# Kernel optimization log

Measured on AMD Instinct MI355X. Metric: run time of the kernel, lower is better.

The kernel has to match this reference:

```python
import jax, jax.numpy as jnp
import numpy as np

K = 12           # boundary_k
TEMP = 0.75      # logit_temperature


def _knn_idx(p):
    # p: [N,3]; brute-force kNN within one batch element (pointops offsets => per-batch)
    sq = jnp.sum(p * p, axis=-1)
    d2 = sq[:, None] + sq[None, :] - 2.0 * (p @ p.T)   # [N,N]
    _, idx = jax.lax.top_k(-d2, K + 1)                  # self is nearest (d=0)
    return idx[:, 1:]                                    # drop self -> [N,K]


def _mlp2(x, W1, b1, W2, b2, relu_out):
    h = jax.nn.relu(x @ W1 + b1) @ W2 + b2
    return jax.nn.relu(h) if relu_out else h


def setup_inputs() -> dict:
    key = jax.random.key(0)
    ks = jax.random.split(key, 32)
    B, N, C = 4, 4096, 17
    dims = [256, 512, 768]
    RD = 320
    s = 0.02
    inp = {
        'feat0': jax.random.normal(ks[0], (B, N, dims[0]), jnp.float32),
        'feat1': jax.random.normal(ks[1], (B, N, dims[1]), jnp.float32),
        'feat2': jax.random.normal(ks[2], (B, N, dims[2]), jnp.float32),
        'logits': jax.random.normal(ks[3], (B, N, C), jnp.float32),
        'labels': jax.random.randint(ks[4], (B, N), 0, C, jnp.int32),
        'pos': jax.random.normal(ks[5], (B, N, 3), jnp.float32),
    }
    # feat projections
    for i, d in enumerate(dims):
        inp[f'Wp{i}'] = jax.random.normal(ks[6 + i], (d, RD), jnp.float32) * s
        inp[f'bp{i}'] = jnp.zeros((RD,), jnp.float32)
    # boundary encoder 6->96->160
    inp['Wbe1'] = jax.random.normal(ks[10], (6, 96), jnp.float32) * s
    inp['bbe1'] = jnp.zeros((96,), jnp.float32)
    inp['Wbe2'] = jax.random.normal(ks[11], (96, 160), jnp.float32) * s
    inp['bbe2'] = jnp.zeros((160,), jnp.float32)
    # attention (RD+160)->320->n_scales
    inp['Wa1'] = jax.random.normal(ks[12], (RD + 160, 320), jnp.float32) * s
    inp['ba1'] = jnp.zeros((320,), jnp.float32)
    inp['Wa2'] = jax.random.normal(ks[13], (320, 3), jnp.float32) * s
    inp['ba2'] = jnp.zeros((3,), jnp.float32)
    # output proj RD->RD->RD
    inp['Wo1'] = jax.random.normal(ks[14], (RD, RD), jnp.float32) * s
    inp['bo1'] = jnp.zeros((RD,), jnp.float32)
    inp['Wo2'] = jax.random.normal(ks[15], (RD, RD), jnp.float32) * s
    inp['bo2'] = jnp.zeros((RD,), jnp.float32)
    return inp


def boundary_info(logits, labels, pos):
    idx = jax.vmap(_knn_idx)(pos)                          # [B,N,K]
    nb_lab = jax.vmap(lambda l, i: l[i])(labels, idx)      # [B,N,K]
    nb_pos = jax.vmap(lambda p, i: p[i])(pos, idx)         # [B,N,K,3]
    diff = nb_lab != labels[..., None]                     # [B,N,K]
    diff_f = diff.astype(jnp.float32)
    dist = jnp.linalg.norm(nb_pos - pos[:, :, None, :], axis=-1)  # [B,N,K]
    boundary_score = diff_f.mean(axis=-1)
    same = 1.0 - diff_f
    same_dist = (dist * same).sum(-1) / (same.sum(-1) + 1e-6)
    bdist = jnp.min(jnp.where(diff, dist, jnp.inf), axis=-1)
    bdist = jnp.where(jnp.isfinite(bdist), bdist, same_dist)
    mean_d = dist.mean(-1)
    density = 1.0 / (mean_d + 1e-6)
    curvature = jnp.std(dist, axis=-1, ddof=1) / (mean_d + 1e-6)  # torch.std unbiased
    probs = jax.nn.softmax(logits / TEMP, axis=-1)
    confidence = probs.max(-1)
    entropy = -(probs * jnp.log(probs + 1e-8)).sum(-1) / jnp.log(jnp.float32(probs.shape[-1]))
    return jnp.stack([boundary_score, confidence, entropy, density, curvature, bdist], axis=-1)


def reference(feat0, feat1, feat2, logits, labels, pos,
              Wp0, bp0, Wp1, bp1, Wp2, bp2,
              Wbe1, bbe1, Wbe2, bbe2,
              Wa1, ba1, Wa2, ba2,
              Wo1, bo1, Wo2, bo2):
    fp = jnp.stack([feat0 @ Wp0 + bp0, feat1 @ Wp1 + bp1, feat2 @ Wp2 + bp2], axis=2)  # [B,N,3,RD]
    info = boundary_info(logits, labels, pos)                       # [B,N,6]
    enc = _mlp2(info, Wbe1, bbe1, Wbe2, bbe2, relu_out=True)        # [B,N,160]
    global_feat = fp.mean(axis=2)                                   # [B,N,RD]
    attn_in = jnp.concatenate([global_feat, enc], axis=-1)
    attn = jax.nn.softmax(_mlp2(attn_in, Wa1, ba1, Wa2, ba2, relu_out=False), axis=-1)  # [B,N,3]
    fused = (fp * attn[..., None]).sum(axis=2)                      # [B,N,RD]
    out = _mlp2(fused, Wo1, bo1, Wo2, bo2, relu_out=False) + global_feat
    return out, attn
```

## Files before the change

kernel.cpp:

```cpp
#include <hip/hip_runtime.h>
#include <stdint.h>

typedef float fx4 __attribute__((ext_vector_type(4)));
typedef short s8 __attribute__((ext_vector_type(8)));
typedef short s4 __attribute__((ext_vector_type(4)));
typedef unsigned int u32;
typedef u32 ux4 __attribute__((ext_vector_type(4)));

#define MTOT 16384
#define NPTS 4096

#define VMCNT3 asm volatile("s_waitcnt vmcnt(3)" ::: "memory")
#define VMCNT2 asm volatile("s_waitcnt vmcnt(2)" ::: "memory")
#define VMCNT0 asm volatile("s_waitcnt vmcnt(0)" ::: "memory")
#define LGKM0  asm volatile("s_waitcnt lgkmcnt(0)" ::: "memory")
#define SBAR   asm volatile("s_barrier" ::: "memory")
#define SCHED0 __builtin_amdgcn_sched_barrier(0)

__device__ __forceinline__ float b2f(short s) {
    return __uint_as_float(((unsigned)(unsigned short)s) << 16);
}
__device__ __forceinline__ short f2b(float f) {
    unsigned u = __float_as_uint(f);
    u += 0x7fffu + ((u >> 16) & 1u);
    return (short)(u >> 16);
}
__device__ __forceinline__ void g2l16(const void* g, void* l) {
    __builtin_amdgcn_global_load_lds(
        (const __attribute__((address_space(1))) unsigned int*)g,
        (__attribute__((address_space(3))) unsigned int*)l, 16, 0, 0);
}
__device__ __forceinline__ void g2l4(const void* g, void* l) {
    __builtin_amdgcn_global_load_lds(
        (const __attribute__((address_space(1))) unsigned int*)g,
        (__attribute__((address_space(3))) unsigned int*)l, 4, 0, 0);
}

struct WTDesc {
    const float* W[8];
    short* Bt[8];
    int K[8];
    int N[8];
    int Kp[8];
    int swz[8];
    int base[9];
};

__global__ __launch_bounds__(256) void wtrans8_kernel(WTDesc d)
{
    int idx = blockIdx.x * 256 + threadIdx.x;
    if (idx >= d.base[8]) return;
    int s = 0;
#pragma unroll
    for (int t = 1; t < 8; ++t) if (idx >= d.base[t]) s = t;
    int local = idx - d.base[s];
    int N = d.N[s];
    if (d.swz[s]) {
        int c = local / 10240, r = local - c * 10240;
        int n = r >> 5, q = r & 31, slot = q >> 3, t = q & 7;
        int kl = ((slot ^ ((n >> 1) & 3)) << 3) | t;
        int k = c * 32 + kl;
        d.Bt[s][local] = f2b(d.W[s][(size_t)k * N + n]);
    } else {
        int Kp = d.Kp[s], K = d.K[s];
        int n = local / Kp, k = local - n * Kp;
        d.Bt[s][local] = (k < K) ? f2b(d.W[s][(size_t)k * N + n]) : (short)0;
    }
}

#define SEGW 132
#define KCAP 40

__global__ __launch_bounds__(512) void knap_kernel(
    const float* __restrict__ pos, u32* __restrict__ keys,
    const float* __restrict__ f0, const float* __restrict__ f1, const float* __restrict__ f2,
    short* __restrict__ a0, short* __restrict__ a1, short* __restrict__ a2)
{
    __shared__ float xs[8 * SEGW], ys[8 * SEGW], zs[8 * SEGW];
    __shared__ u32 cand[64 * KCAP];
    __shared__ u32 samp[64 * 16];
    __shared__ u32 tauA[64];
    __shared__ int cnt[64];

    if (blockIdx.x >= 1024) {
        int g = (blockIdx.x - 1024) * 512 + threadIdx.x;
        const float* src; short* dst; int K; size_t w;
        if (g < 1572864)      { src = f2; dst = a2; K = 768; w = (size_t)g * 8; }
        else if (g < 2621440) { src = f1; dst = a1; K = 512; w = (size_t)(g - 1572864) * 8; }
        else                  { src = f0; dst = a0; K = 256; w = (size_t)(g - 2621440) * 8; }
        int Kt = K * 64;
        int mtile = (int)(w / (size_t)Kt);
        int r2 = (int)(w - (size_t)mtile * Kt);
        int chunk = r2 >> 11;
        int within = r2 & 2047;
        int r = within >> 5, q = within & 31;
        int slot = q >> 3;
        int k = chunk * 32 + ((slot ^ ((r >> 1) & 3)) << 3);
        int row = mtile * 64 + r;
        const float* sp = src + (size_t)row * K + k;
        fx4 v0 = *(const fx4*)sp, v1 = *(const fx4*)(sp + 4);
        s8 o;
        o[0] = f2b(v0[0]); o[1] = f2b(v0[1]); o[2] = f2b(v0[2]); o[3] = f2b(v0[3]);
        o[4] = f2b(v1[0]); o[5] = f2b(v1[1]); o[6] = f2b(v1[2]); o[7] = f2b(v1[3]);
        *(s8*)(dst + w) = o;
        return;
    }

    int bid = blockIdx.x;
    int b   = bid >> 8;
    int cc  = (bid >> 6) & 3;
    int pch = bid & 63;
    int tid = threadIdx.x;
    int jb  = cc << 10;

    if (tid < 64) cnt[tid] = 0;
    for (int idx = tid; idx < 1024; idx += 512) {
        int seg = idx >> 7, o = idx & 127;
        const float* pp = pos + (size_t)(b * NPTS + jb + idx) * 3;
        xs[seg * SEGW + o] = pp[0];
        ys[seg * SEGW + o] = pp[1];
        zs[seg * SEGW + o] = pp[2];
    }
    __syncthreads();

    int lp = tid >> 3, q = tid & 7;
    int gi = pch * 64 + lp;
    const float* mp = pos + (size_t)(b * NPTS + gi) * 3;
    float mx = mp[0], my = mp[1], mz = mp[2];

    const float* xsq = xs + q * SEGW;
    const float* ysq = ys + q * SEGW;
    const float* zsq = zs + q * SEGW;
    int jg0 = jb + q * 128;

    u32 h0 = 0xFFFFFFFFu, h1v = 0xFFFFFFFFu;
    for (int jj = 0; jj < 128; jj += 4) {
        fx4 xv = *reinterpret_cast<const fx4*>(xsq + jj);
        fx4 yv = *reinterpret_cast<const fx4*>(ysq + jj);
        fx4 zv = *reinterpret_cast<const fx4*>(zsq + jj);
#pragma unroll
        for (int u = 0; u < 4; ++u) {
            float dx = xv[u] - mx, dy = yv[u] - my, dz = zv[u] - mz;
            float d2 = fmaf(dx, dx, fmaf(dy, dy, dz * dz));
            int jg = jg0 + jj + u;
            u32 key = (__float_as_uint(d2) & 0xFFFFF000u) | (u32)jg;
            if (jg == gi) key = 0xFFFFFFFFu;
            u32 lo = (key < h0) ? key : h0;
            u32 hi = (key < h0) ? h0 : key;
            h0 = lo;
            h1v = (hi < h1v) ? hi : h1v;
        }
    }
    samp[lp * 16 + q * 2]     = h0;
    samp[lp * 16 + q * 2 + 1] = h1v;
    __syncthreads();

    {
        ux4 sv0 = *(ux4*)&samp[lp * 16];
        ux4 sv1 = *(ux4*)&samp[lp * 16 + 4];
        ux4 sv2 = *(ux4*)&samp[lp * 16 + 8];
        ux4 sv3 = *(ux4*)&samp[lp * 16 + 12];
        int r0 = 0, r1 = 0;
#pragma unroll
        for (int i = 0; i < 4; ++i) {
            r0 += (sv0[i] < h0) + (sv1[i] < h0) + (sv2[i] < h0) + (sv3[i] < h0);
            r1 += (sv0[i] < h1v) + (sv1[i] < h1v) + (sv2[i] < h1v) + (sv3[i] < h1v);
        }
        if (r0 == 11) tauA[lp] = h0;
        if (r1 == 11) tauA[lp] = h1v;
    }
    __syncthreads();
    u32 tau = tauA[lp];

    for (int jj = 0; jj < 128; jj += 4) {
        fx4 xv = *reinterpret_cast<const fx4*>(xsq + jj);
        fx4 yv = *reinterpret_cast<const fx4*>(ysq + jj);
        fx4 zv = *reinterpret_cast<const fx4*>(zsq + jj);
#pragma unroll
        for (int u = 0; u < 4; ++u) {
            float dx = xv[u] - mx, dy = yv[u] - my, dz = zv[u] - mz;
            float d2 = fmaf(dx, dx, fmaf(dy, dy, dz * dz));
            int jg = jg0 + jj + u;
            u32 key = (__float_as_uint(d2) & 0xFFFFF000u) | (u32)jg;
            if (jg == gi) key = 0xFFFFFFFFu;
            if (key <= tau) {
                int slot = atomicAdd(&cnt[lp], 1);
                if (slot < KCAP) cand[lp * KCAP + slot] = key;
            }
        }
    }
    __syncthreads();

    int n = cnt[lp];
    u32 out[12];
    if (n <= KCAP) {
        u32 e0, e1, e2, e3, e4;
        e0 = (q      < n) ? cand[lp * KCAP + q]      : 0xFFFFFFFFu;
        e1 = (q + 8  < n) ? cand[lp * KCAP + q + 8]  : 0xFFFFFFFFu;
        e2 = (q + 16 < n) ? cand[lp * KCAP + q + 16] : 0xFFFFFFFFu;
        e3 = (q + 24 < n) ? cand[lp * KCAP + q + 24] : 0xFFFFFFFFu;
        e4 = (q + 32 < n) ? cand[lp * KCAP + q + 32] : 0xFFFFFFFFu;
#define CE(a, b) { u32 t0 = (a < b) ? a : b; u32 t1 = (a < b) ? b : a; a = t0; b = t1; }
        CE(e0, e1) CE(e1, e2) CE(e2, e3) CE(e3, e4)
        CE(e0, e1) CE(e1, e2) CE(e2, e3)
        CE(e0, e1) CE(e1, e2)
        CE(e0, e1)
#undef CE
        cand[lp * KCAP + q]      = e0;
        cand[lp * KCAP + q + 8]  = e1;
        cand[lp * KCAP + q + 16] = e2;
        cand[lp * KCAP + q + 24] = e3;
        cand[lp * KCAP + q + 32] = e4;
        int ptr = 0;
        u32 head = e0;
#pragma unroll
        for (int r = 0; r < 12; ++r) {
            u32 m = head;
            u32 o1 = __shfl_xor(m, 4, 8); m = (o1 < m) ? o1 : m;
            u32 o2 = __shfl_xor(m, 2, 8); m = (o2 < m) ? o2 : m;
            u32 o3 = __shfl_xor(m, 1, 8); m = (o3 < m) ? o3 : m;
            if (m == head) {
                ++ptr;
                head = (ptr < 5) ? cand[lp * KCAP + q + ptr * 8] : 0xFFFFFFFFu;
            }
            out[r] = m;
        }
    } else {
        u32 hk[12];
#pragma unroll
        for (int k = 0; k < 12; ++k) hk[k] = 0xFFFFFFFFu;
        for (int jj = 0; jj < 128; jj += 4) {
            fx4 xv = *reinterpret_cast<const fx4*>(xsq + jj);
            fx4 yv = *reinterpret_cast<const fx4*>(ysq + jj);
            fx4 zv = *reinterpret_cast<const fx4*>(zsq + jj);
#pragma unroll
            for (int u = 0; u < 4; ++u) {
                float dx = xv[u] - mx, dy = yv[u] - my, dz = zv[u] - mz;
                float d2 = fmaf(dx, dx, fmaf(dy, dy, dz * dz));
                int jg = jg0 + jj + u;
                u32 key = (__float_as_uint(d2) & 0xFFFFF000u) | (u32)jg;
                if (jg == gi) key = 0xFFFFFFFFu;
                if (key < hk[11]) {
                    hk[11] = key;
#pragma unroll
                    for (int k = 11; k >= 1; --k) {
                        u32 a = hk[k], bb = hk[k - 1];
                        u32 mn = (a < bb) ? a : bb;
                        u32 mxv = (a < bb) ? bb : a;
                        hk[k - 1] = mn; hk[k] = mxv;
                    }
                }
            }
        }
#pragma unroll
        for (int r = 0; r < 12; ++r) {
            u32 m = hk[0];
            u32 o1 = __shfl_xor(m, 4, 8); m = (o1 < m) ? o1 : m;
            u32 o2 = __shfl_xor(m, 2, 8); m = (o2 < m) ? o2 : m;
            u32 o3 = __shfl_xor(m, 1, 8); m = (o3 < m) ? o3 : m;
            if (m == hk[0]) {
#pragma unroll
                for (int k = 0; k < 11; ++k) hk[k] = hk[k + 1];
                hk[11] = 0xFFFFFFFFu;
            }
            out[r] = m;
        }
    }

    size_t kb = ((size_t)(b * NPTS + gi) * 4 + cc) * 12;
    if (q == 0) *reinterpret_cast<ux4*>(&keys[kb])     = (ux4){out[0], out[1], out[2], out[3]};
    if (q == 1) *reinterpret_cast<ux4*>(&keys[kb + 4]) = (ux4){out[4], out[5], out[6], out[7]};
    if (q == 2) *reinterpret_cast<ux4*>(&keys[kb + 8]) = (ux4){out[8], out[9], out[10], out[11]};
}

__global__ __launch_bounds__(256) void knn_merge_kernel(
    const u32* __restrict__ keys, const int* __restrict__ labels,
    const float* __restrict__ logits, float* __restrict__ info32)
{
    __shared__ unsigned char labs[NPTS];
    int b  = blockIdx.x >> 6;
    int pc = blockIdx.x & 63;
    int tid = threadIdx.x;
    for (int idx = tid; idx < NPTS; idx += 256)
        labs[idx] = (unsigned char)labels[b * NPTS + idx];
    __syncthreads();

    int lp = tid >> 2, q = tid & 3;
    int gi = pc * 64 + lp;
    size_t kb = ((size_t)(b * NPTS + gi) * 4 + q) * 12;
    ux4 k0 = *reinterpret_cast<const ux4*>(&keys[kb]);
    ux4 k1 = *reinterpret_cast<const ux4*>(&keys[kb + 4]);
    ux4 k2 = *reinterpret_cast<const ux4*>(&keys[kb + 8]);
    u32 hk[12];
    hk[0] = k0[0]; hk[1] = k0[1]; hk[2] = k0[2]; hk[3] = k0[3];
    hk[4] = k1[0]; hk[5] = k1[1]; hk[6] = k1[2]; hk[7] = k1[3];
    hk[8] = k2[0]; hk[9] = k2[1]; hk[10] = k2[2]; hk[11] = k2[3];

    int mylab = (int)labs[gi];
    float sum_d = 0.f, sum_d2 = 0.f, sum_diff = 0.f, same_d = 0.f, bmin = 3.0e38f;
#pragma unroll
    for (int r = 0; r < 12; ++r) {
        u32 m = hk[0];
        u32 o1 = __shfl_xor(m, 2, 4); m = (o1 < m) ? o1 : m;
        u32 o2 = __shfl_xor(m, 1, 4); m = (o2 < m) ? o2 : m;
        if (m == hk[0]) {
#pragma unroll
            for (int k = 0; k < 11; ++k) hk[k] = hk[k + 1];
            hk[11] = 0xFFFFFFFFu;
        }
        float d = sqrtf(__uint_as_float(m & 0xFFFFF000u));
        int j = (int)(m & 0xFFFu);
        float isdiff = ((int)labs[j] != mylab) ? 1.0f : 0.0f;
        sum_d += d;
        sum_d2 = fmaf(d, d, sum_d2);
        sum_diff += isdiff;
        same_d = fmaf(d, 1.0f - isdiff, same_d);
        if (isdiff > 0.f) bmin = fminf(bmin, d);
    }

    if (q == 0) {
        float nsame = 12.0f - sum_diff;
        float mean_d = sum_d * (1.0f / 12.0f);
        float var = fmaxf(0.f, (sum_d2 - 12.0f * mean_d * mean_d) * (1.0f / 11.0f));
        float md_eps = mean_d + 1e-6f;
        float curvature = sqrtf(var) / md_eps;
        float density = 1.0f / md_eps;
        float same_dist = same_d / (nsame + 1e-6f);
        float bdist = (bmin < 2.9e38f) ? bmin : same_dist;
        float bscore = sum_diff * (1.0f / 12.0f);

        const float* lg = logits + (size_t)(b * NPTS + gi) * 17;
        float v[17];
        float vmax = -3.0e38f;
#pragma unroll
        for (int c = 0; c < 17; ++c) { v[c] = lg[c] * (1.0f / 0.75f); vmax = fmaxf(vmax, v[c]); }
        float ssum = 0.f;
#pragma unroll
        for (int c = 0; c < 17; ++c) { v[c] = expf(v[c] - vmax); ssum += v[c]; }
        float inv = 1.0f / ssum;
        float conf = 0.f, ent = 0.f;
#pragma unroll
        for (int c = 0; c < 17; ++c) {
            float pprob = v[c] * inv;
            conf = fmaxf(conf, pprob);
            ent += pprob * logf(pprob + 1e-8f);
        }
        ent = -ent * (1.0f / 2.8332133f);

        float* op = info32 + (size_t)(b * NPTS + gi) * 32;
        fx4 o0 = {bscore, conf, ent, density};
        fx4 o1v = {curvature, bdist, 0.f, 0.f};
        fx4 zz = {0.f, 0.f, 0.f, 0.f};
        *reinterpret_cast<fx4*>(op + 0)  = o0;
        *reinterpret_cast<fx4*>(op + 4)  = o1v;
        *reinterpret_cast<fx4*>(op + 8)  = zz;
        *reinterpret_cast<fx4*>(op + 12) = zz;
        *reinterpret_cast<fx4*>(op + 16) = zz;
        *reinterpret_cast<fx4*>(op + 20) = zz;
        *reinterpret_cast<fx4*>(op + 24) = zz;
        *reinterpret_cast<fx4*>(op + 28) = zz;
    }
}

template<bool AF32, bool RELU, bool NMASK, bool ADDF, bool OUTF, bool OUTB>
__global__ __launch_bounds__(256) void gemm_k(
    const void* __restrict__ Ap, int lda,
    const short* __restrict__ Bt,
    const float* __restrict__ bias,
    float* __restrict__ Cf, int ldcf,
    short* __restrict__ Cb, int ldcb, int cboff,
    const float* __restrict__ Af, int ldaf,
    int N, int K, int ntiles)
{
    __shared__ short As[128 * 40];
    __shared__ short Bs[64 * 40];
    int bid = blockIdx.x;
    int mt = bid / ntiles, nt = bid - mt * ntiles;
    int m0 = mt * 128, n0 = nt * 64;
    int tid = threadIdx.x, l = tid & 63, wid = tid >> 6;
    int wm = wid & 1, wn = wid >> 1, lr = l & 15, lh = l >> 4;
    fx4 acc[4][2] = {};

    int nsteps = K >> 5;
    for (int kt = 0; kt < nsteps; ++kt) {
        int k0 = kt << 5;
        if constexpr (AF32) {
            const float* A = (const float*)Ap;
#pragma unroll
            for (int it = 0; it < 4; ++it) {
                int tt = tid + it * 256;
                int row = tt >> 3, seg = tt & 7;
                fx4 vv = *reinterpret_cast<const fx4*>(A + (size_t)(m0 + row) * lda + k0 + seg * 4);
                s4 w; w[0] = f2b(vv[0]); w[1] = f2b(vv[1]); w[2] = f2b(vv[2]); w[3] = f2b(vv[3]);
                *reinterpret_cast<s4*>(&As[row * 40 + seg * 4]) = w;
            }
        } else {
            const short* A = (const short*)Ap;
#pragma unroll
            for (int it = 0; it < 2; ++it) {
                int tt = tid + it * 256;
                int row = tt >> 2, seg = tt & 3;
                s8 vv = *reinterpret_cast<const s8*>(A + (size_t)(m0 + row) * lda + k0 + seg * 8);
                *reinterpret_cast<s8*>(&As[row * 40 + seg * 8]) = vv;
            }
        }
        {
            int row = tid >> 2, seg = tid & 3;
            s8 vb = {0, 0, 0, 0, 0, 0, 0, 0};
            if (!NMASK || (n0 + row) < N)
                vb = *reinterpret_cast<const s8*>(Bt + (size_t)(n0 + row) * K + k0 + seg * 8);
            *reinterpret_cast<s8*>(&Bs[row * 40 + seg * 8]) = vb;
        }
        __syncthreads();
        s8 af[4], bfr[2];
#pragma unroll
        for (int mf = 0; mf < 4; ++mf)
            af[mf] = *reinterpret_cast<s8*>(&As[(wm * 64 + mf * 16 + lr) * 40 + lh * 8]);
#pragma unroll
        for (int nf = 0; nf < 2; ++nf)
            bfr[nf] = *reinterpret_cast<s8*>(&Bs[(wn * 32 + nf * 16 + lr) * 40 + lh * 8]);
#pragma unroll
        for (int mf = 0; mf < 4; ++mf)
#pragma unroll
            for (int nf = 0; nf < 2; ++nf)
                acc[mf][nf] = __builtin_amdgcn_mfma_f32_16x16x32_bf16(af[mf], bfr[nf], acc[mf][nf], 0, 0, 0);
        __syncthreads();
    }

#pragma unroll
    for (int nf = 0; nf < 2; ++nf) {
        int col = n0 + wn * 32 + nf * 16 + lr;
        if (NMASK && col >= N) continue;
        float bv = bias[col];
#pragma unroll
        for (int mf = 0; mf < 4; ++mf) {
            int r0 = m0 + wm * 64 + mf * 16 + lh * 4;
#pragma unroll
            for (int rg = 0; rg < 4; ++rg) {
                float c = acc[mf][nf][rg] + bv;
                if (RELU) c = fmaxf(c, 0.0f);
                int row = r0 + rg;
                if constexpr (ADDF) c += Af[(size_t)row * ldaf + col];
                if constexpr (OUTF) Cf[(size_t)row * ldcf + col] = c;
                if constexpr (OUTB) Cb[(size_t)row * ldcb + cboff + col] = f2b(c);
            }
        }
    }
}

__global__ __launch_bounds__(1024, 1) void mega_kernel(
    const short* __restrict__ at0, const short* __restrict__ at1, const short* __restrict__ at2,
    const short* __restrict__ btp0, const short* __restrict__ btp1, const short* __restrict__ btp2,
    const float* __restrict__ bp0, const float* __restrict__ bp1, const float* __restrict__ bp2,
    const short* __restrict__ bta1, const float* __restrict__ ba1,
    const float* __restrict__ Wa2, const float* __restrict__ ba2,
    const short* __restrict__ bto1, const float* __restrict__ bo1,
    const short* __restrict__ bto2, const float* __restrict__ bo2,
    const short* __restrict__ encb,
    float* __restrict__ outf, float* __restrict__ attn_out)
{
    __shared__ alignas(16) char smb[136192];
    const int BBo[3] = {0, 20480, 40960};
    const int ABo[3] = {61440, 65536, 69632};
    constexpr int R2B = 73728, SWF = 135168;
    float* smf = (float*)(smb + SWF);

    int tid = threadIdx.x, wid = tid >> 6, l = tid & 63;
    int wm = wid >> 2, wn = wid & 3, lr = l & 15, lh = l >> 4;
    int m0 = blockIdx.x * 64;

    auto stageB = [&](int bbase, const short* btg, int kt) {
        const char* s = (const char*)(btg + (size_t)kt * 10240);
        int o1 = tid * 16;
        int o2 = 16384 + tid * 4;
        g2l16(s + o1, smb + bbase + o1);
        g2l4(s + o2, smb + bbase + o2);
    };
    auto stageA = [&](int abase, const short* atgm, int kt) {
        const char* s = (const char*)(atgm + (size_t)kt * 2048);
        g2l4(s + tid * 4, smb + abase + tid * 4);
    };
    auto readB = [&](int bbase, s8* bf) {
#pragma unroll
        for (int nf = 0; nf < 5; ++nf) {
            int row = wn * 80 + nf * 16 + lr;
            bf[nf] = *(const s8*)(smb + bbase + row * 64 + ((lh ^ ((row >> 1) & 3)) << 4));
        }
    };

    fx4 gacc[5] = {};

    auto do_proj = [&](const short* atgm, const short* btg, int ns,
                       const float* bias, s4 (&fpks)[5]) {
        fx4 acc[5] = {};
        stageB(BBo[0], btg, 0); stageA(ABo[0], atgm, 0);
        stageB(BBo[1], btg, 1); stageA(ABo[1], atgm, 1);
        LGKM0;
#pragma unroll 1
        for (int kt = 0; kt < ns; ++kt) {
            if (kt < ns - 1) { VMCNT3; } else { VMCNT0; }
            SBAR;
            int ph = kt - (kt / 3) * 3;
            s8 af, bf[5];
            {
                int row = wm * 16 + lr;
                af = *(const s8*)(smb + ABo[ph] + row * 64 + ((lh ^ ((row >> 1) & 3)) << 4));
            }
            readB(BBo[ph], bf);
            if (kt + 2 < ns) {
                int p2 = (kt + 2) - ((kt + 2) / 3) * 3;
                stageB(BBo[p2], btg, kt + 2);
                stageA(ABo[p2], atgm, kt + 2);
            }
#pragma unroll
            for (int nf = 0; nf < 5; ++nf)
                acc[nf] = __builtin_amdgcn_mfma_f32_16x16x32_bf16(af, bf[nf], acc[nf], 0, 0, 0);
            SCHED0; LGKM0;
        }
        SBAR;
#pragma unroll
        for (int nf = 0; nf < 5; ++nf) {
            float bv = bias[wn * 80 + nf * 16 + lr];
            s4 pk;
#pragma unroll
            for (int rg = 0; rg < 4; ++rg) {
                float c = acc[nf][rg] + bv;
                gacc[nf][rg] += c;
                pk[rg] = f2b(c);
            }
            fpks[nf] = pk;
        }
    };

    s4 fpk0[5], fpk1[5], fpk2[5];
    do_proj(at2 + (size_t)blockIdx.x * 49152, btp2, 24, bp2, fpk2);
    do_proj(at1 + (size_t)blockIdx.x * 32768, btp1, 16, bp1, fpk1);
    do_proj(at0 + (size_t)blockIdx.x * 16384, btp0, 8,  bp0, fpk0);

    s4 gh[5];
#pragma unroll
    for (int nf = 0; nf < 5; ++nf) {
        int col = wn * 80 + nf * 16 + lr;
        s4 pk;
#pragma unroll
        for (int rg = 0; rg < 4; ++rg) {
            int row = wm * 16 + lh * 4 + rg;
            short gs = f2b(gacc[nf][rg] * (1.0f / 3.0f));
            pk[rg] = gs;
            int bir = (col * 2) ^ (((row >> 1) & 3) << 4);
            *(short*)(smb + R2B + row * 960 + bir) = gs;
        }
        gh[nf] = pk;
    }
#pragma unroll
    for (int r = 0; r < 2; ++r) {
        int idx = tid + r * 1024;
        if (idx < 1280) {
            int row = idx / 20, sg = idx - row * 20;
            s8 v = *reinterpret_cast<const s8*>(encb + (size_t)(m0 + row) * 160 + sg * 8);
            int bir = (640 + sg * 16) ^ (((row >> 1) & 3) << 4);
            *(s8*)(smb + R2B + row * 960 + bir) = v;
        }
    }

    auto do_gemm2 = [&](const short* btg, int ns, fx4 (&acc)[5]) {
        stageB(BBo[0], btg, 0);
        stageB(BBo[1], btg, 1);
        LGKM0;
#pragma unroll 1
        for (int kt = 0; kt < ns; ++kt) {
            if (kt < ns - 1) { VMCNT2; } else { VMCNT0; }
            SBAR;
            int ph = kt - (kt / 3) * 3;
            s8 af, bf[5];
            {
                int row = wm * 16 + lr;
                int bir = (kt * 64 + (lh << 4)) ^ (((row >> 1) & 3) << 4);
                af = *(const s8*)(smb + R2B + row * 960 + bir);
            }
            readB(BBo[ph], bf);
            if (kt + 2 < ns) {
                int p2 = (kt + 2) - ((kt + 2) / 3) * 3;
                stageB(BBo[p2], btg, kt + 2);
            }
#pragma unroll
            for (int nf = 0; nf < 5; ++nf)
                acc[nf] = __builtin_amdgcn_mfma_f32_16x16x32_bf16(af, bf[nf], acc[nf], 0, 0, 0);
            SCHED0; LGKM0;
        }
        SBAR;
    };

    {
        fx4 acc1[5] = {};
        do_gemm2(bta1, 15, acc1);
#pragma unroll
        for (int nf = 0; nf < 5; ++nf) {
            int col = wn * 80 + nf * 16 + lr;
            float bv = ba1[col];
#pragma unroll
            for (int rg = 0; rg < 4; ++rg) {
                int row = wm * 16 + lh * 4 + rg;
                int bir = (col * 2) ^ (((row >> 1) & 3) << 4);
                *(short*)(smb + R2B + row * 960 + bir) = f2b(fmaxf(acc1[nf][rg] + bv, 0.0f));
            }
        }
    }

    {
        float* ws2 = (float*)smb;
        if (tid < 240)
            reinterpret_cast<fx4*>(ws2)[tid] = reinterpret_cast<const fx4*>(Wa2)[tid];
        __syncthreads();
        if (tid < 512) {
            int row = tid >> 3, g = tid & 7;
            float l0 = 0.f, l1 = 0.f, l2 = 0.f;
#pragma unroll
            for (int j = 0; j < 5; ++j) {
                int bir = (g * 80 + j * 16) ^ (((row >> 1) & 3) << 4);
                s8 v = *(const s8*)(smb + R2B + row * 960 + bir);
#pragma unroll
                for (int u = 0; u < 8; ++u) {
                    float f = b2f(v[u]);
                    const float* wp = ws2 + (g * 40 + j * 8 + u) * 3;
                    l0 = fmaf(f, wp[0], l0);
                    l1 = fmaf(f, wp[1], l1);
                    l2 = fmaf(f, wp[2], l2);
                }
            }
#pragma unroll
            for (int s = 4; s >= 1; s >>= 1) {
                l0 += __shfl_xor(l0, s, 8);
                l1 += __shfl_xor(l1, s, 8);
                l2 += __shfl_xor(l2, s, 8);
            }
            if (g == 0) {
                l0 += ba2[0]; l1 += ba2[1]; l2 += ba2[2];
                float mx = fmaxf(l0, fmaxf(l1, l2));
                float e0 = expf(l0 - mx), e1 = expf(l1 - mx), e2 = expf(l2 - mx);
                float inv = 1.0f / (e0 + e1 + e2);
                float w0 = e0 * inv, w1 = e1 * inv, w2 = e2 * inv;
                attn_out[(size_t)(m0 + row) * 3 + 0] = w0;
                attn_out[(size_t)(m0 + row) * 3 + 1] = w1;
                attn_out[(size_t)(m0 + row) * 3 + 2] = w2;
                smf[row * 4 + 0] = w0; smf[row * 4 + 1] = w1; smf[row * 4 + 2] = w2;
            }
        }
        __syncthreads();
    }

#pragma unroll
    for (int rg = 0; rg < 4; ++rg) {
        int row = wm * 16 + lh * 4 + rg;
        float w0 = smf[row * 4 + 0], w1 = smf[row * 4 + 1], w2 = smf[row * 4 + 2];
#pragma unroll
        for (int nf = 0; nf < 5; ++nf) {
            int col = wn * 80 + nf * 16 + lr;
            float fv = w0 * b2f(fpk0[nf][rg])
                     + w1 * b2f(fpk1[nf][rg])
                     + w2 * b2f(fpk2[nf][rg]);
            int bir = (col * 2) ^ (((row >> 1) & 3) << 4);
            *(short*)(smb + R2B + row * 960 + bir) = f2b(fv);
        }
    }

    {
        fx4 acch[5] = {};
        do_gemm2(bto1, 10, acch);
#pragma unroll
        for (int nf = 0; nf < 5; ++nf) {
            int col = wn * 80 + nf * 16 + lr;
            float bv = bo1[col];
#pragma unroll
            for (int rg = 0; rg < 4; ++rg) {
                int row = wm * 16 + lh * 4 + rg;
                int bir = (col * 2) ^ (((row >> 1) & 3) << 4);
                *(short*)(smb + R2B + row * 960 + bir) = f2b(fmaxf(acch[nf][rg] + bv, 0.0f));
            }
        }
    }

    {
        fx4 acco[5] = {};
        do_gemm2(bto2, 10, acco);
#pragma unroll
        for (int nf = 0; nf < 5; ++nf) {
            int col = wn * 80 + nf * 16 + lr;
            float bv = bo2[col];
#pragma unroll
            for (int rg = 0; rg < 4; ++rg) {
                int row = m0 + wm * 16 + lh * 4 + rg;
                float c = acco[nf][rg] + bv + b2f(gh[nf][rg]);
                outf[(size_t)row * 320 + col] = c;
            }
        }
    }
}

extern "C" void kernel_launch(void* const* d_in, const int* in_sizes, int n_in,
                              void* d_out, int out_size, void* d_ws, size_t ws_size,
                              hipStream_t stream)
{
    const float* feat0  = (const float*)d_in[0];
    const float* feat1  = (const float*)d_in[1];
    const float* feat2  = (const float*)d_in[2];
    const float* logits = (const float*)d_in[3];
    const int*   labels = (const int*)d_in[4];
    const float* pos    = (const float*)d_in[5];
    const float* Wp0 = (const float*)d_in[6];   const float* bp0 = (const float*)d_in[7];
    const float* Wp1 = (const float*)d_in[8];   const float* bp1 = (const float*)d_in[9];
    const float* Wp2 = (const float*)d_in[10];  const float* bp2 = (const float*)d_in[11];
    const float* Wbe1 = (const float*)d_in[12]; const float* bbe1 = (const float*)d_in[13];
    const float* Wbe2 = (const float*)d_in[14]; const float* bbe2 = (const float*)d_in[15];
    const float* Wa1 = (const float*)d_in[16];  const float* ba1 = (const float*)d_in[17];
    const float* Wa2 = (const float*)d_in[18];  const float* ba2 = (const float*)d_in[19];
    const float* Wo1 = (const float*)d_in[20];  const float* bo1 = (const float*)d_in[21];
    const float* Wo2 = (const float*)d_in[22];  const float* bo2 = (const float*)d_in[23];

    char* p = (char*)d_ws;
    auto alloc = [&](size_t bytes) { char* r = p; p += (bytes + 255) & ~(size_t)255; return r; };
    short* bt_p0  = (short*)alloc((size_t)320 * 256 * 2);
    short* bt_p1  = (short*)alloc((size_t)320 * 512 * 2);
    short* bt_p2  = (short*)alloc((size_t)320 * 768 * 2);
    short* bt_be1 = (short*)alloc((size_t)96 * 32 * 2);
    short* bt_be2 = (short*)alloc((size_t)160 * 96 * 2);
    short* bt_a1  = (short*)alloc((size_t)320 * 480 * 2);
    short* bt_o1  = (short*)alloc((size_t)320 * 320 * 2);
    short* bt_o2  = (short*)alloc((size_t)320 * 320 * 2);
    float* info32 = (float*)alloc((size_t)MTOT * 32 * 4);
    short* h1     = (short*)alloc((size_t)MTOT * 96 * 2);
    short* encb   = (short*)alloc((size_t)MTOT * 160 * 2);
    u32*   knnkeys= (u32*)alloc((size_t)MTOT * 4 * 12 * 4);
    short* abt0   = (short*)alloc((size_t)MTOT * 256 * 2);
    short* abt1   = (short*)alloc((size_t)MTOT * 512 * 2);
    short* abt2   = (short*)alloc((size_t)MTOT * 768 * 2);

    float* outf = (float*)d_out;
    float* attn_out = outf + (size_t)MTOT * 320;

    WTDesc wd;
    const float* Ws[8] = {Wp0, Wp1, Wp2, Wbe1, Wbe2, Wa1, Wo1, Wo2};
    short* Bts[8] = {bt_p0, bt_p1, bt_p2, bt_be1, bt_be2, bt_a1, bt_o1, bt_o2};
    int Ks[8]  = {256, 512, 768, 6, 96, 480, 320, 320};
    int Ns[8]  = {320, 320, 320, 96, 160, 320, 320, 320};
    int Kps[8] = {256, 512, 768, 32, 96, 480, 320, 320};
    int Sz[8]  = {1, 1, 1, 0, 0, 1, 1, 1};
    int acc = 0;
    for (int s = 0; s < 8; ++s) {
        wd.W[s] = Ws[s]; wd.Bt[s] = Bts[s];
        wd.K[s] = Ks[s]; wd.N[s] = Ns[s]; wd.Kp[s] = Kps[s]; wd.swz[s] = Sz[s];
        wd.base[s] = acc;
        acc += Ns[s] * Kps[s];
    }
    wd.base[8] = acc;
    wtrans8_kernel<<<(acc + 255) / 256, 256, 0, stream>>>(wd);

    knap_kernel<<<7168, 512, 0, stream>>>(pos, knnkeys,
                                          feat0, feat1, feat2,
                                          abt0, abt1, abt2);
    knn_merge_kernel<<<256, 256, 0, stream>>>(knnkeys, labels, logits, info32);

    gemm_k<true, true, true, false, false, true><<<256, 256, 0, stream>>>(
        info32, 32, bt_be1, bbe1, nullptr, 0, h1, 96, 0, nullptr, 0, 96, 32, 2);
    gemm_k<false, true, true, false, false, true><<<384, 256, 0, stream>>>(
        h1, 96, bt_be2, bbe2, nullptr, 0, encb, 160, 0, nullptr, 0, 160, 96, 3);

    mega_kernel<<<256, 1024, 0, stream>>>(
        abt0, abt1, abt2,
        bt_p0, bt_p1, bt_p2,
        bp0, bp1, bp2,
        bt_a1, ba1, Wa2, ba2,
        bt_o1, bo1, bt_o2, bo2,
        encb, outf, attn_out);
}
```

Before: 158.1 us.

## Halve mega_kernel row tile to 32 with 512 threads and LDS-staged projections

The fused projection/attention/output kernel now processes 32 rows per block with 512 threads across 512 blocks, instead of 64 rows with 1024 threads across 256 blocks. The feature pre-swizzle is retiled to 32-row tiles to match. Each thread now issues more B-tile loads, so the vmcnt waits are raised. The three per-scale projection results are kept in shared memory rather than registers, which raises LDS use to about 160KB. The aim is to spread work over more CUs (256 blocks underfill the device) and lower register pressure. The cost is reloading the full weight tiles for twice as many blocks.

```diff
diff --git a/kernel.cpp b/kernel.cpp
--- a/kernel.cpp
+++ b/kernel.cpp
@@ -10,8 +10,8 @@
 #define MTOT 16384
 #define NPTS 4096
 
-#define VMCNT3 asm volatile("s_waitcnt vmcnt(3)" ::: "memory")
-#define VMCNT2 asm volatile("s_waitcnt vmcnt(2)" ::: "memory")
+#define VMCNT5 asm volatile("s_waitcnt vmcnt(5)" ::: "memory")
+#define VMCNT4 asm volatile("s_waitcnt vmcnt(4)" ::: "memory")
 #define VMCNT0 asm volatile("s_waitcnt vmcnt(0)" ::: "memory")
 #define LGKM0  asm volatile("s_waitcnt lgkmcnt(0)" ::: "memory")
 #define SBAR   asm volatile("s_barrier" ::: "memory")
@@ -88,15 +88,15 @@
         if (g < 1572864)      { src = f2; dst = a2; K = 768; w = (size_t)g * 8; }
         else if (g < 2621440) { src = f1; dst = a1; K = 512; w = (size_t)(g - 1572864) * 8; }
         else                  { src = f0; dst = a0; K = 256; w = (size_t)(g - 2621440) * 8; }
-        int Kt = K * 64;
+        int Kt = K * 32;
         int mtile = (int)(w / (size_t)Kt);
         int r2 = (int)(w - (size_t)mtile * Kt);
-        int chunk = r2 >> 11;
-        int within = r2 & 2047;
+        int chunk = r2 >> 10;
+        int within = r2 & 1023;
         int r = within >> 5, q = within & 31;
         int slot = q >> 3;
         int k = chunk * 32 + ((slot ^ ((r >> 1) & 3)) << 3);
-        int row = mtile * 64 + r;
+        int row = mtile * 32 + r;
         const float* sp = src + (size_t)row * K + k;
         fx4 v0 = *(const fx4*)sp, v1 = *(const fx4*)(sp + 4);
         s8 o;
@@ -448,7 +448,7 @@
     }
 }
 
-__global__ __launch_bounds__(1024, 1) void mega_kernel(
+__global__ __launch_bounds__(512, 1) void mega_kernel(
     const short* __restrict__ at0, const short* __restrict__ at1, const short* __restrict__ at2,
     const short* __restrict__ btp0, const short* __restrict__ btp1, const short* __restrict__ btp2,
     const float* __restrict__ bp0, const float* __restrict__ bp1, const float* __restrict__ bp2,
@@ -459,25 +459,30 @@
     const short* __restrict__ encb,
     float* __restrict__ outf, float* __restrict__ attn_out)
 {
-    __shared__ alignas(16) char smb[136192];
+    __shared__ alignas(16) char smb[160256];
     const int BBo[3] = {0, 20480, 40960};
-    const int ABo[3] = {61440, 65536, 69632};
-    constexpr int R2B = 73728, SWF = 135168;
+    const int ABo[3] = {61440, 63488, 65536};
+    const int FPo[3] = {67584, 88064, 108544};
+    constexpr int R2B = 129024, SWF = 159744;
     float* smf = (float*)(smb + SWF);
 
     int tid = threadIdx.x, wid = tid >> 6, l = tid & 63;
     int wm = wid >> 2, wn = wid & 3, lr = l & 15, lh = l >> 4;
-    int m0 = blockIdx.x * 64;
+    int m0 = blockIdx.x * 32;
 
     auto stageB = [&](int bbase, const short* btg, int kt) {
         const char* s = (const char*)(btg + (size_t)kt * 10240);
         int o1 = tid * 16;
-        int o2 = 16384 + tid * 4;
+        int o2 = 8192 + tid * 16;
+        int o3 = 16384 + tid * 4;
+        int o4 = 18432 + tid * 4;
         g2l16(s + o1, smb + bbase + o1);
-        g2l4(s + o2, smb + bbase + o2);
+        g2l16(s + o2, smb + bbase + o2);
+        g2l4(s + o3, smb + bbase + o3);
+        g2l4(s + o4, smb + bbase + o4);
     };
     auto stageA = [&](int abase, const short* atgm, int kt) {
-        const char* s = (const char*)(atgm + (size_t)kt * 2048);
+        const char* s = (const char*)(atgm + (size_t)kt * 1024);
         g2l4(s + tid * 4, smb + abase + tid * 4);
     };
     auto readB = [&](int bbase, s8* bf) {
@@ -491,14 +496,14 @@
     fx4 gacc[5] = {};
 
     auto do_proj = [&](const short* atgm, const short* btg, int ns,
-                       const float* bias, s4 (&fpks)[5]) {
+                       const float* bias, int fpbase) {
         fx4 acc[5] = {};
         stageB(BBo[0], btg, 0); stageA(ABo[0], atgm, 0);
         stageB(BBo[1], btg, 1); stageA(ABo[1], atgm, 1);
         LGKM0;
 #pragma unroll 1
         for (int kt = 0; kt < ns; ++kt) {
-            if (kt < ns - 1) { VMCNT3; } else { VMCNT0; }
+            if (kt < ns - 1) { VMCNT5; } else { VMCNT0; }
             SBAR;
             int ph = kt - (kt / 3) * 3;
             s8 af, bf[5];
@@ -520,22 +525,22 @@
         SBAR;
 #pragma unroll
         for (int nf = 0; nf < 5; ++nf) {
-            float bv = bias[wn * 80 + nf * 16 + lr];
-            s4 pk;
+            int col = wn * 80 + nf * 16 + lr;
+            float bv = bias[col];
 #pragma unroll
             for (int rg = 0; rg < 4; ++rg) {
+                int row = wm * 16 + lh * 4 + rg;
                 float c = acc[nf][rg] + bv;
                 gacc[nf][rg] += c;
-                pk[rg] = f2b(c);
-            }
-            fpks[nf] = pk;
+                int bir = (col * 2) ^ (((row >> 1) & 3) << 4);
+                *(short*)(smb + fpbase + row * 640 + bir) = f2b(c);
+            }
         }
     };
 
-    s4 fpk0[5], fpk1[5], fpk2[5];
-    do_proj(at2 + (size_t)blockIdx.x * 49152, btp2, 24, bp2, fpk2);
-    do_proj(at1 + (size_t)blockIdx.x * 32768, btp1, 16, bp1, fpk1);
-    do_proj(at0 + (size_t)blockIdx.x * 16384, btp0, 8,  bp0, fpk0);
+    do_proj(at2 + (size_t)blockIdx.x * 24576, btp2, 24, bp2, FPo[2]);
+    do_proj(at1 + (size_t)blockIdx.x * 16384, btp1, 16, bp1, FPo[1]);
+    do_proj(at0 + (size_t)blockIdx.x * 8192,  btp0, 8,  bp0, FPo[0]);
 
     s4 gh[5];
 #pragma unroll
@@ -554,8 +559,8 @@
     }
 #pragma unroll
     for (int r = 0; r < 2; ++r) {
-        int idx = tid + r * 1024;
-        if (idx < 1280) {
+        int idx = tid + r * 512;
+        if (idx < 640) {
             int row = idx / 20, sg = idx - row * 20;
             s8 v = *reinterpret_cast<const s8*>(encb + (size_t)(m0 + row) * 160 + sg * 8);
             int bir = (640 + sg * 16) ^ (((row >> 1) & 3) << 4);
@@ -569,7 +574,7 @@
         LGKM0;
 #pragma unroll 1
         for (int kt = 0; kt < ns; ++kt) {
-            if (kt < ns - 1) { VMCNT2; } else { VMCNT0; }
+            if (kt < ns - 1) { VMCNT4; } else { VMCNT0; }
             SBAR;
             int ph = kt - (kt / 3) * 3;
             s8 af, bf[5];
@@ -612,7 +617,7 @@
         if (tid < 240)
             reinterpret_cast<fx4*>(ws2)[tid] = reinterpret_cast<const fx4*>(Wa2)[tid];
         __syncthreads();
-        if (tid < 512) {
+        if (tid < 256) {
             int row = tid >> 3, g = tid & 7;
             float l0 = 0.f, l1 = 0.f, l2 = 0.f;
 #pragma unroll
@@ -656,10 +661,10 @@
 #pragma unroll
         for (int nf = 0; nf < 5; ++nf) {
             int col = wn * 80 + nf * 16 + lr;
-            float fv = w0 * b2f(fpk0[nf][rg])
-                     + w1 * b2f(fpk1[nf][rg])
-                     + w2 * b2f(fpk2[nf][rg]);
             int bir = (col * 2) ^ (((row >> 1) & 3) << 4);
+            float fv = w0 * b2f(*(const short*)(smb + FPo[0] + row * 640 + bir))
+                     + w1 * b2f(*(const short*)(smb + FPo[1] + row * 640 + bir))
+                     + w2 * b2f(*(const short*)(smb + FPo[2] + row * 640 + bir));
             *(short*)(smb + R2B + row * 960 + bir) = f2b(fv);
         }
     }
@@ -765,7 +770,7 @@
     gemm_k<false, true, true, false, false, true><<<384, 256, 0, stream>>>(
         h1, 96, bt_be2, bbe2, nullptr, 0, encb, 160, 0, nullptr, 0, 160, 96, 3);
 
-    mega_kernel<<<256, 1024, 0, stream>>>(
+    mega_kernel<<<512, 512, 0, stream>>>(
         abt0, abt1, abt2,
         bt_p0, bt_p1, bt_p2,
         bp0, bp1, bp2,
```

Measured after the change: 165.9 us. +5.0%, slower.
